# Optimization experiments

Measured on AMD Instinct MI355X. Metric: run time of the kernel, lower is better.

Reference implementation:

```python
import jax, jax.numpy as jnp
import numpy as np

N_NODES = 20000
N_EDGES = 200000
NUM_GRAPHS = 512
IN_C = 16      # in_channel
P1 = 128       # edge MLP hidden
P2 = 16        # base channel width
F_E = 16       # nbr_edge_features
C1_OUT = 3 * P2  # 48
C2_OUT = 2 * P2  # 32
C3_OUT = P2      # 16


def _nnconv(x, src, tgt, ea, W1, b1, W2, b2, root, bias, in_c, out_c):
    # edge MLP -> per-edge weight matrix [E, in_c, out_c]
    h = jax.nn.relu(ea @ W1 + b1)
    We = (h @ W2 + b2).reshape(-1, in_c, out_c)
    msg = jnp.einsum('ei,eio->eo', x[src], We)          # gather + batched matmul
    n = x.shape[0]
    agg = jax.ops.segment_sum(msg, tgt, num_segments=n)  # scatter
    deg = jax.ops.segment_sum(jnp.ones((src.shape[0],), x.dtype), tgt, num_segments=n)
    agg = agg / jnp.maximum(deg, 1.0)[:, None]           # aggr='mean'
    return agg + x @ root + bias


def _set2set(x, batch, Wih, Whh, bih, bhh, num_graphs, steps=2):
    H = x.shape[-1]
    q_star = jnp.zeros((num_graphs, 2 * H), x.dtype)
    h = jnp.zeros((num_graphs, H), x.dtype)
    c = jnp.zeros_like(h)
    for _ in range(steps):
        gates = q_star @ Wih.T + bih + h @ Whh.T + bhh   # LSTM cell (i,f,g,o)
        i, f, g, o = jnp.split(gates, 4, axis=-1)
        c = jax.nn.sigmoid(f) * c + jax.nn.sigmoid(i) * jnp.tanh(g)
        h = jax.nn.sigmoid(o) * jnp.tanh(c)
        e = jnp.sum(x * h[batch], axis=-1)               # attention logits per node
        emax = jax.ops.segment_max(e, batch, num_segments=num_graphs)
        a = jnp.exp(e - jnp.maximum(emax, -1e30)[batch])
        asum = jax.ops.segment_sum(a, batch, num_segments=num_graphs)
        a = a / jnp.maximum(asum, 1e-16)[batch]
        r = jax.ops.segment_sum(a[:, None] * x, batch, num_segments=num_graphs)
        q_star = jnp.concatenate([h, r], axis=-1)
    return q_star


def setup_inputs() -> dict:
    key = jax.random.key(0)
    ks = iter(jax.random.split(key, 40))
    d = {}
    d['x'] = jax.random.normal(next(ks), (N_NODES, IN_C), jnp.float32)
    d['edge_index'] = jax.random.randint(next(ks), (2, N_EDGES), 0, N_NODES)
    d['edge_attr'] = jax.random.uniform(next(ks), (N_EDGES, F_E), jnp.float32)
    d['batch'] = jnp.sort(jax.random.randint(next(ks), (N_NODES,), 0, NUM_GRAPHS))

    def lin(ki, fan_in, fan_out):
        s = 1.0 / np.sqrt(fan_in)
        return jax.random.uniform(ki, (fan_in, fan_out), jnp.float32, -s, s)

    for name, ic, oc in [('c1', IN_C, C1_OUT), ('c2', C1_OUT, C2_OUT), ('c3', C2_OUT, C3_OUT)]:
        d[name + '_W1'] = lin(next(ks), F_E, P1)
        d[name + '_b1'] = jnp.zeros((P1,), jnp.float32)
        d[name + '_W2'] = lin(next(ks), P1, ic * oc) * 0.1
        d[name + '_b2'] = jnp.zeros((ic * oc,), jnp.float32)
        d[name + '_root'] = lin(next(ks), ic, oc)
        d[name + '_bias'] = jnp.zeros((oc,), jnp.float32)

    H = P2
    s = 1.0 / np.sqrt(H)
    d['lstm_Wih'] = jax.random.uniform(next(ks), (4 * H, 2 * H), jnp.float32, -s, s)
    d['lstm_Whh'] = jax.random.uniform(next(ks), (4 * H, H), jnp.float32, -s, s)
    d['lstm_bih'] = jnp.zeros((4 * H,), jnp.float32)
    d['lstm_bhh'] = jnp.zeros((4 * H,), jnp.float32)

    tot = 2 * P2
    d['lin1_W'] = lin(next(ks), tot, tot // 2)
    d['lin1_b'] = jnp.zeros((tot // 2,), jnp.float32)
    d['lin2_W'] = lin(next(ks), tot // 2, tot // 4)
    d['lin2_b'] = jnp.zeros((tot // 4,), jnp.float32)
    d['linf_W'] = lin(next(ks), tot // 4, 1)
    d['linf_b'] = jnp.zeros((1,), jnp.float32)
    return d


def reference(x, edge_index, edge_attr, batch,
              c1_W1, c1_b1, c1_W2, c1_b2, c1_root, c1_bias,
              c2_W1, c2_b1, c2_W2, c2_b2, c2_root, c2_bias,
              c3_W1, c3_b1, c3_W2, c3_b2, c3_root, c3_bias,
              lstm_Wih, lstm_Whh, lstm_bih, lstm_bhh,
              lin1_W, lin1_b, lin2_W, lin2_b, linf_W, linf_b):
    src, tgt = edge_index[0], edge_index[1]
    y = jax.nn.relu(_nnconv(x, src, tgt, edge_attr, c1_W1, c1_b1, c1_W2, c1_b2, c1_root, c1_bias, IN_C, C1_OUT))
    y = jax.nn.relu(_nnconv(y, src, tgt, edge_attr, c2_W1, c2_b1, c2_W2, c2_b2, c2_root, c2_bias, C1_OUT, C2_OUT))
    y = jax.nn.relu(_nnconv(y, src, tgt, edge_attr, c3_W1, c3_b1, c3_W2, c3_b2, c3_root, c3_bias, C2_OUT, C3_OUT))
    y = _set2set(y, batch, lstm_Wih, lstm_Whh, lstm_bih, lstm_bhh, NUM_GRAPHS, steps=2)  # [B, 2*P2]
    y = jax.nn.relu(y @ lin1_W + lin1_b)
    y = jax.nn.relu(y @ lin2_W + lin2_b)
    y = (y @ linf_W + linf_b).squeeze(-1)  # [B]
    return y
```

## Files before the change

### kernel.cpp

```cpp
#include <hip/hip_runtime.h>

#define NN 20000
#define NE 200000
#define NG 512

typedef float v2f __attribute__((ext_vector_type(2)));

__device__ __forceinline__ int lowerb(const int* a, int n, int v){
  int lo=0, hi=n;
  while(lo<hi){ int m=(lo+hi)>>1; if(a[m]<v) lo=m+1; else hi=m; }
  return lo;
}

template<int AUX>
__device__ __forceinline__ void gload_lds16(const float4* g, float4* l){
  __builtin_amdgcn_global_load_lds(
    (const __attribute__((address_space(1))) void*)(g),
    (__attribute__((address_space(3))) void*)(l), 16, 0, AUX);
}

__global__ void k_count(const int* __restrict__ tgt, int* __restrict__ cnt){
  int e = blockIdx.x*blockDim.x + threadIdx.x;
  if(e<NE) atomicAdd(&cnt[tgt[e]], 1);
}

__global__ void k_scan(const int* __restrict__ cnt, int* __restrict__ row_start){
  __shared__ int part[1024];
  int t = threadIdx.x;
  const int CH = (NN + 1023)/1024;
  int i0 = t*CH;
  int s = 0;
  for(int j=0;j<CH;j++){ int i=i0+j; if(i<NN) s += cnt[i]; }
  part[t] = s; __syncthreads();
  for(int d=1; d<1024; d<<=1){
    int v = (t>=d) ? part[t-d] : 0;
    __syncthreads();
    part[t] += v;
    __syncthreads();
  }
  int run = (t==0) ? 0 : part[t-1];
  for(int j=0;j<CH;j++){ int i=i0+j; if(i<NN){ row_start[i]=run; run += cnt[i]; } }
  if(t==0) row_start[NN] = part[1023];
}

__global__ void k_place(const int* __restrict__ src, const int* __restrict__ tgt,
                        const float* __restrict__ ea,
                        const int* __restrict__ row_start, int* __restrict__ cur,
                        int* __restrict__ es_src, float* __restrict__ es_ea){
  int e = blockIdx.x*blockDim.x + threadIdx.x;
  if(e>=NE) return;
  int n = tgt[e];
  int pos = row_start[n] + atomicAdd(&cur[n],1);
  es_src[pos] = src[e];
  const float4* s = (const float4*)ea + (size_t)e*4;
  float4* d = (float4*)es_ea + (size_t)pos*4;
  d[0]=s[0]; d[1]=s[1]; d[2]=s[2]; d[3]=s[3];
}

template<int IC, int OC, int PLEN, int KS, int BN, int PP, int TI, int OQ, int TO, bool PF, int EB>
__launch_bounds__(256, 3)
__global__ void k_layer(const float* __restrict__ x_in, const float* __restrict__ es_ea,
                        const int* __restrict__ es_src, const int* __restrict__ row_start,
                        const float* __restrict__ W1, const float* __restrict__ b1,
                        const float* __restrict__ W2, float* __restrict__ part,
                        float* __restrict__ xbar_out)
{
  constexpr int K    = PLEN*IC;
  constexpr int XV   = IC/4;
  constexpr int NIW  = IC/TI;
  constexpr int NPW  = PLEN/PP;
  constexpr int G    = BN/4;
  constexpr int KQL  = 64/OQ;
  constexpr int TSPL = 4*KQL;
  constexpr int J    = (K/4)/TSPL;
  constexpr int NEA  = EB/64;
  constexpr int NX4  = (EB*XV)/256;
  constexpr int TI2  = TI/2;
  constexpr int NP   = TO/2;
  constexpr bool TODD = (TO & 1);
  constexpr int EPB  = 256/PLEN;
  static_assert(TI%2==0, "packed scatter needs even TI");
  static_assert(256%PLEN==0, "H-compute mapping");
  static_assert(EB%64==0, "ea region must be exact 256-f4 chunks");
  static_assert((EB*XV)%256==0, "xs region must be exact 256-f4 chunks");
  static_assert(EB*(PLEN+16+IC) <= BN*K, "staging alias fits in S");
  static_assert(NPW*NIW==64, "wave tile covers 64 lanes");
  static_assert(G*PP*TI <= 48, "spill-safe accumulator");
  static_assert(OQ*TO==OC && (K/4)%TSPL==0, "gemm tiling");
  static_assert(J%2==0, "ping-pong needs even J");

  __shared__ __align__(16) float S[BN*K];
  __shared__ int rs_s[BN+1], ro[BN+1];

  float* hb  = S;
  float* eas = S + EB*PLEN;
  float* xs  = S + EB*(PLEN+16);

  const int tid = threadIdx.x;
  const int wid = tid>>6, lane = tid&63;
  const int split = blockIdx.x % KS;
  const int nb = blockIdx.x / KS;
  const int n0 = nb*BN;

  if(tid<=BN) rs_s[tid] = row_start[n0+tid];
  __syncthreads();
  const int estart = rs_s[0], eend = rs_s[BN];

  const int pw = lane / NIW;
  const int iw = lane - pw*NIW;
  const int pcol = tid % PLEN, erow = tid / PLEN;

  float w1c[16];
  const float b1c = b1[split*PLEN + pcol];
  #pragma unroll
  for(int i=0;i<16;i++) w1c[i] = W1[i*128 + split*PLEN + pcol];

  v2f acc2[G][PP][TI2];
  v2f xsum2[G][TI2];
  #pragma unroll
  for(int g=0;g<G;g++){
    #pragma unroll
    for(int p=0;p<PP;p++)
      #pragma unroll
      for(int u=0;u<TI2;u++) acc2[g][p][u]=v2f{0.f,0.f};
    #pragma unroll
    for(int u=0;u<TI2;u++) xsum2[g][u]=v2f{0.f,0.f};
  }

  const float4* EA4 = (const float4*)es_ea;
  const float4* x4  = (const float4*)x_in;

  for(int bstart=estart; bstart<eend; bstart+=EB){
    const int ebc = min(EB, eend-bstart);
    if(tid<=BN){ int v = rs_s[tid]-bstart; ro[tid] = min(max(v,0), ebc); }
    const int ea_lim = ebc*4, xs_lim = ebc*XV;
    int sn_r[NX4];
    #pragma unroll
    for(int c=0;c<NX4;c++){
      int jc = min(tid + c*256, xs_lim-1);
      sn_r[c] = es_src[bstart + jc/XV];
    }
    #pragma unroll
    for(int c=0;c<NEA;c++){
      int j = tid + c*256;
      int jc = min(j, ea_lim-1);
      gload_lds16<0>(EA4 + (size_t)bstart*4 + jc, ((float4*)eas) + j);
    }
    #pragma unroll
    for(int c=0;c<NX4;c++){
      int j = tid + c*256;
      int jc = min(j, xs_lim-1);
      int q = jc - (jc/XV)*XV;
      gload_lds16<0>(x4 + (size_t)sn_r[c]*XV + q, ((float4*)xs) + j);
    }
    __syncthreads();

    for(int ec = erow; ec < ebc; ec += EPB){
      float h = b1c;
      #pragma unroll
      for(int q=0;q<4;q++){
        float4 a = *(const float4*)&eas[ec*16 + 4*q];
        h += a.x*w1c[4*q] + a.y*w1c[4*q+1] + a.z*w1c[4*q+2] + a.w*w1c[4*q+3];
      }
      hb[ec*PLEN + pcol] = fmaxf(h, 0.f);
    }
    __syncthreads();

    if constexpr (PF){
      #pragma unroll
      for(int g=0; g<G; g++){
        const int nl = wid*G + g;
        const int a = ro[nl], b = ro[nl+1];
        if(a>=b) continue;
        float hv[PP]; v2f xv2[TI2];
        #pragma unroll
        for(int p=0;p<PP;p++) hv[p] = hb[a*PLEN + pw*PP + p];
        #pragma unroll
        for(int u=0;u<TI2;u++) xv2[u] = *(const v2f*)&xs[a*IC + iw*TI + 2*u];
        for(int e=a; e<b; e++){
          float hn[PP]; v2f xn2[TI2];
          if(e+1<b){
            #pragma unroll
            for(int p=0;p<PP;p++) hn[p] = hb[(e+1)*PLEN + pw*PP + p];
            #pragma unroll
            for(int u=0;u<TI2;u++) xn2[u] = *(const v2f*)&xs[(e+1)*IC + iw*TI + 2*u];
          }
          #pragma unroll
          for(int p=0;p<PP;p++){
            v2f h2 = v2f{hv[p], hv[p]};
            #pragma unroll
            for(int u=0;u<TI2;u++) acc2[g][p][u] += h2*xv2[u];
          }
          #pragma unroll
          for(int u=0;u<TI2;u++) xsum2[g][u] += xv2[u];
          #pragma unroll
          for(int p=0;p<PP;p++) hv[p]=hn[p];
          #pragma unroll
          for(int u=0;u<TI2;u++) xv2[u]=xn2[u];
        }
      }
    } else {
      #pragma unroll
      for(int g=0; g<G; g++){
        const int nl = wid*G + g;
        const int a = ro[nl], b = ro[nl+1];
        for(int e=a; e<b; e++){
          float hv[PP];
          #pragma unroll
          for(int p=0;p<PP;p++) hv[p] = hb[e*PLEN + pw*PP + p];
          v2f xv2[TI2];
          #pragma unroll
          for(int u=0;u<TI2;u++) xv2[u] = *(const v2f*)&xs[e*IC + iw*TI + 2*u];
          #pragma unroll
          for(int p=0;p<PP;p++){
            v2f h2 = v2f{hv[p], hv[p]};
            #pragma unroll
            for(int u=0;u<TI2;u++) acc2[g][p][u] += h2*xv2[u];
          }
          #pragma unroll
          for(int u=0;u<TI2;u++) xsum2[g][u] += xv2[u];
        }
      }
    }
    __syncthreads();
  }

  if(split==0 && pw==0){
    #pragma unroll
    for(int g=0;g<G;g++){
      const int nl = wid*G + g;
      const float dv = 1.f/fmaxf((float)(rs_s[nl+1]-rs_s[nl]), 1.f);
      #pragma unroll
      for(int u=0;u<TI2;u++){
        v2f r = xsum2[g][u]*v2f{dv,dv};
        *(v2f*)&xbar_out[(size_t)(n0+nl)*IC + iw*TI + 2*u] = r;
      }
    }
  }

  #pragma unroll
  for(int g=0; g<G; g++){
    const int nl = wid*G + g;
    const float dv = 1.f/fmaxf((float)(rs_s[nl+1]-rs_s[nl]), 1.f);
    const v2f dv2 = v2f{dv, dv};
    #pragma unroll
    for(int p=0;p<PP;p++)
      #pragma unroll
      for(int u=0;u<TI2;u++)
        *(v2f*)&S[(nl*PLEN + pw*PP + p)*IC + iw*TI + 2*u] = acc2[g][p][u]*dv2;
  }

  const int oq  = lane % OQ;
  const int kql = lane / OQ;
  const int o0  = oq*TO;
  const float* W2b = W2 + (size_t)split*K*OC + o0;

  auto LOADW = [&](int j, v2f (&wv2)[4][NP], float (&wvs)[4]){
    const int k4 = j*TSPL + wid*KQL + kql;
    #pragma unroll
    for(int r=0;r<4;r++){
      const float* wr = W2b + (size_t)(4*k4+r)*OC;
      if constexpr (TO==4){
        float4 a=*(const float4*)wr;
        wv2[r][0]=v2f{a.x,a.y}; wv2[r][1]=v2f{a.z,a.w};
      } else if constexpr (TO==3){
        wv2[r][0]=v2f{wr[0],wr[1]}; wvs[r]=wr[2];
      } else {
        float2 a=*(const float2*)wr;
        wv2[r][0]=v2f{a.x,a.y};
      }
    }
  };

  v2f outp2[BN][NP];
  float outs[BN];
  #pragma unroll
  for(int n=0;n<BN;n++){
    #pragma unroll
    for(int t=0;t<NP;t++) outp2[n][t]=v2f{0.f,0.f};
    outs[n]=0.f;
  }

  v2f wvA[4][NP], wvB[4][NP];
  float wsA[4], wsB[4];
  LOADW(0, wvA, wsA);
  __syncthreads();

  #pragma unroll 1
  for(int j=0;j<J;j+=2){
    LOADW(j+1, wvB, wsB);
    {
      const int k4 = j*TSPL + wid*KQL + kql;
      #pragma unroll
      for(int n=0;n<BN;n++){
        float4 sv = *(const float4*)&S[n*K + 4*k4];
        v2f s0=v2f{sv.x,sv.x}, s1=v2f{sv.y,sv.y}, s2=v2f{sv.z,sv.z}, s3=v2f{sv.w,sv.w};
        #pragma unroll
        for(int t=0;t<NP;t++)
          outp2[n][t] += s0*wvA[0][t] + s1*wvA[1][t] + s2*wvA[2][t] + s3*wvA[3][t];
        if constexpr (TODD)
          outs[n] += sv.x*wsA[0] + sv.y*wsA[1] + sv.z*wsA[2] + sv.w*wsA[3];
      }
    }
    if(j+2<J) LOADW(j+2, wvA, wsA);
    {
      const int k4 = (j+1)*TSPL + wid*KQL + kql;
      #pragma unroll
      for(int n=0;n<BN;n++){
        float4 sv = *(const float4*)&S[n*K + 4*k4];
        v2f s0=v2f{sv.x,sv.x}, s1=v2f{sv.y,sv.y}, s2=v2f{sv.z,sv.z}, s3=v2f{sv.w,sv.w};
        #pragma unroll
        for(int t=0;t<NP;t++)
          outp2[n][t] += s0*wvB[0][t] + s1*wvB[1][t] + s2*wvB[2][t] + s3*wvB[3][t];
        if constexpr (TODD)
          outs[n] += sv.x*wsB[0] + sv.y*wsB[1] + sv.z*wsB[2] + sv.w*wsB[3];
      }
    }
  }

  #pragma unroll
  for(int m=OQ; m<64; m<<=1)
    #pragma unroll
    for(int n=0;n<BN;n++){
      #pragma unroll
      for(int t=0;t<NP;t++){
        outp2[n][t][0] += __shfl_xor(outp2[n][t][0], m, 64);
        outp2[n][t][1] += __shfl_xor(outp2[n][t][1], m, 64);
      }
      if constexpr (TODD) outs[n] += __shfl_xor(outs[n], m, 64);
    }

  if(kql==0){
    float* slice = part + (size_t)(split*4+wid)*NN*OC;
    #pragma unroll
    for(int n=0;n<BN;n++){
      float* dst = slice + (size_t)(n0+n)*OC + o0;
      if constexpr (TO==4){
        *(float4*)dst = make_float4(outp2[n][0][0],outp2[n][0][1],outp2[n][1][0],outp2[n][1][1]);
      } else if constexpr (TO==3){
        dst[0]=outp2[n][0][0]; dst[1]=outp2[n][0][1]; dst[2]=outs[n];
      } else {
        *(float2*)dst = make_float2(outp2[n][0][0],outp2[n][0][1]);
      }
    }
  }
}

template<int IC, int OC, int SL>
__global__ void k_epi(const float* __restrict__ part, const float* __restrict__ x,
                      const float* __restrict__ xbar,
                      const float* __restrict__ root, const float* __restrict__ b2,
                      const float* __restrict__ bias, float* __restrict__ y)
{
  for(int idx = blockIdx.x*256 + threadIdx.x; idx < NN*OC; idx += gridDim.x*256){
    int n = idx/OC, o = idx - n*OC;
    float v = bias[o];
    #pragma unroll
    for(int s=0;s<SL;s++) v += part[(size_t)s*NN*OC + idx];
    #pragma unroll
    for(int i=0;i<IC;i++) v += x[(size_t)n*IC+i]*root[i*OC+o];
    #pragma unroll
    for(int i=0;i<IC;i++) v += xbar[(size_t)n*IC+i]*b2[i*OC+o];
    y[idx] = fmaxf(v, 0.f);
  }
}

__global__ void k_s2s(const float* __restrict__ xg, const int* __restrict__ batch,
  const float* __restrict__ Wih, const float* __restrict__ Whh,
  const float* __restrict__ bih, const float* __restrict__ bhh,
  const float* __restrict__ l1W, const float* __restrict__ l1b,
  const float* __restrict__ l2W, const float* __restrict__ l2b,
  const float* __restrict__ lfW, const float* __restrict__ lfb,
  float* __restrict__ out)
{
  int g = blockIdx.x, lane = threadIdx.x;
  __shared__ float hs[16], cs[16], qs[32], gs[64], rs[16];
  int r0 = lowerb(batch, NN, g);
  int r1 = lowerb(batch, NN, g+1);
  if(lane<16){ hs[lane]=0.f; cs[lane]=0.f; }
  if(lane<32) qs[lane]=0.f;
  __syncthreads();
  for(int step=0; step<2; step++){
    float gate = bih[lane] + bhh[lane];
    for(int k=0;k<32;k++) gate += qs[k]*Wih[lane*32+k];
    for(int k=0;k<16;k++) gate += hs[k]*Whh[lane*16+k];
    gs[lane] = gate;
    __syncthreads();
    if(lane<16){
      float ig = 1.f/(1.f+expf(-gs[lane]));
      float fg = 1.f/(1.f+expf(-gs[lane+16]));
      float gg = tanhf(gs[lane+32]);
      float og = 1.f/(1.f+expf(-gs[lane+48]));
      float cn = fg*cs[lane] + ig*gg;
      cs[lane] = cn;
      hs[lane] = og*tanhf(cn);
    }
    __syncthreads();
    float m = -1e30f;
    for(int n=r0+lane; n<r1; n+=64){
      float e=0.f;
      for(int k=0;k<16;k++) e += xg[n*16+k]*hs[k];
      m = fmaxf(m, e);
    }
    for(int d=1; d<64; d<<=1) m = fmaxf(m, __shfl_xor(m, d));
    float ssum = 0.f;
    float racc[16];
    #pragma unroll
    for(int k=0;k<16;k++) racc[k]=0.f;
    for(int n=r0+lane; n<r1; n+=64){
      float e=0.f, xv[16];
      #pragma unroll
      for(int k=0;k<16;k++){ xv[k]=xg[n*16+k]; e += xv[k]*hs[k]; }
      float a = expf(e - m);
      ssum += a;
      #pragma unroll
      for(int k=0;k<16;k++) racc[k] += a*xv[k];
    }
    for(int d=1; d<64; d<<=1) ssum += __shfl_xor(ssum, d);
    #pragma unroll
    for(int k=0;k<16;k++)
      for(int d=1; d<64; d<<=1) racc[k] += __shfl_xor(racc[k], d);
    ssum = fmaxf(ssum, 1e-16f);
    if(lane==0){
      #pragma unroll
      for(int k=0;k<16;k++) rs[k] = racc[k]/ssum;
    }
    __syncthreads();
    if(lane<16){ qs[lane]=hs[lane]; qs[16+lane]=rs[lane]; }
    __syncthreads();
  }
  if(lane<16){
    float v = l1b[lane];
    for(int k=0;k<32;k++) v += qs[k]*l1W[k*16+lane];
    gs[lane] = fmaxf(v,0.f);
  }
  __syncthreads();
  if(lane<8){
    float v = l2b[lane];
    for(int k=0;k<16;k++) v += gs[k]*l2W[k*8+lane];
    gs[32+lane] = fmaxf(v,0.f);
  }
  __syncthreads();
  if(lane==0){
    float v = lfb[0];
    for(int k=0;k<8;k++) v += gs[32+k]*lfW[k];
    out[g] = v;
  }
}

extern "C" void kernel_launch(void* const* d_in, const int* in_sizes, int n_in,
                              void* d_out, int out_size, void* d_ws, size_t ws_size,
                              hipStream_t stream) {
  const float* x0   = (const float*)d_in[0];
  const int*   ei   = (const int*)d_in[1];
  const float* ea   = (const float*)d_in[2];
  const int*   batch= (const int*)d_in[3];
  const float* c1W1 = (const float*)d_in[4];  const float* c1b1 = (const float*)d_in[5];
  const float* c1W2 = (const float*)d_in[6];  const float* c1b2 = (const float*)d_in[7];
  const float* c1rt = (const float*)d_in[8];  const float* c1bs = (const float*)d_in[9];
  const float* c2W1 = (const float*)d_in[10]; const float* c2b1 = (const float*)d_in[11];
  const float* c2W2 = (const float*)d_in[12]; const float* c2b2 = (const float*)d_in[13];
  const float* c2rt = (const float*)d_in[14]; const float* c2bs = (const float*)d_in[15];
  const float* c3W1 = (const float*)d_in[16]; const float* c3b1 = (const float*)d_in[17];
  const float* c3W2 = (const float*)d_in[18]; const float* c3b2 = (const float*)d_in[19];
  const float* c3rt = (const float*)d_in[20]; const float* c3bs = (const float*)d_in[21];
  const float* Wih  = (const float*)d_in[22]; const float* Whh  = (const float*)d_in[23];
  const float* bih  = (const float*)d_in[24]; const float* bhh  = (const float*)d_in[25];
  const float* l1W  = (const float*)d_in[26]; const float* l1b  = (const float*)d_in[27];
  const float* l2W  = (const float*)d_in[28]; const float* l2b  = (const float*)d_in[29];
  const float* lfW  = (const float*)d_in[30]; const float* lfb  = (const float*)d_in[31];
  float* out = (float*)d_out;

  const int* src = ei;
  const int* tgt = ei + NE;

  char* w = (char*)d_ws;
  auto carve = [&](size_t bytes)->void*{ void* p = (void*)w; w += (bytes + 255) & ~(size_t)255; return p; };
  int*   row_start = (int*)carve((NN+1)*sizeof(int));
  int*   cur       = (int*)carve(NN*sizeof(int));
  int*   es_src    = (int*)carve(NE*sizeof(int));
  float* es_ea     = (float*)carve((size_t)NE*16*sizeof(float));
  float* xbar      = (float*)carve((size_t)NN*48*sizeof(float));
  float* y1   = (float*)carve((size_t)NN*48*sizeof(float));
  float* y2   = (float*)carve((size_t)NN*32*sizeof(float));
  float* y3   = (float*)carve((size_t)NN*16*sizeof(float));
  float* part = (float*)carve((size_t)16*NN*48*sizeof(float));

  hipMemsetAsync(cur, 0, NN*sizeof(int), stream);
  k_count<<<(NE+255)/256, 256, 0, stream>>>(tgt, cur);
  k_scan<<<1, 1024, 0, stream>>>(cur, row_start);
  hipMemsetAsync(cur, 0, NN*sizeof(int), stream);
  k_place<<<(NE+255)/256, 256, 0, stream>>>(src, tgt, ea, row_start, cur, es_src, es_ea);

  k_layer<16,48,64,2,8,4,4,16,3,true,64><<<(NN/8)*2, 256, 0, stream>>>(
      x0, es_ea, es_src, row_start, c1W1, c1b1, c1W2, part, xbar);
  k_epi<16,48,8><<<2048, 256, 0, stream>>>(part, x0, xbar, c1rt, c1b2, c1bs, y1);

  k_layer<48,32,32,4,8,4,6,8,4,true,128><<<(NN/8)*4, 256, 0, stream>>>(
      y1, es_ea, es_src, row_start, c2W1, c2b1, c2W2, part, xbar);
  k_epi<48,32,16><<<2048, 256, 0, stream>>>(part, y1, xbar, c2rt, c2b2, c2bs, y2);

  k_layer<32,16,64,2,4,4,8,4,4,true,64><<<(NN/4)*2, 256, 0, stream>>>(
      y2, es_ea, es_src, row_start, c3W1, c3b1, c3W2, part, xbar);
  k_epi<32,16,8><<<2048, 256, 0, stream>>>(part, y2, xbar, c3rt, c3b2, c3bs, y3);

  k_s2s<<<NG, 64, 0, stream>>>(y3, batch, Wih, Whh, bih, bhh, l1W, l1b, l2W, l2b, lfW, lfb, out);
}
```

Before: 723.5 us.

## Combine per-wave partials in LDS and pack edge-MLP hidden compute into v2f

Each block's four waves now reduce their per-node output partials through shared memory before one wave writes a single slice to global memory. This cuts the partial buffer and the epilogue's slice reads by a factor of four (8→2, 16→4, 8→2). The edge MLP hidden layer is also computed two columns per thread with packed float2 FMAs. The cost is two extra block barriers plus LDS traffic at the end of each layer kernel.

```diff
diff --git a/kernel.cpp b/kernel.cpp
--- a/kernel.cpp
+++ b/kernel.cpp
@@ -78,9 +78,10 @@
   constexpr int TI2  = TI/2;
   constexpr int NP   = TO/2;
   constexpr bool TODD = (TO & 1);
-  constexpr int EPB  = 256/PLEN;
+  constexpr int HP   = PLEN/2;
+  constexpr int EPB2 = 256/HP;
   static_assert(TI%2==0, "packed scatter needs even TI");
-  static_assert(256%PLEN==0, "H-compute mapping");
+  static_assert(256%HP==0, "packed H-compute mapping");
   static_assert(EB%64==0, "ea region must be exact 256-f4 chunks");
   static_assert((EB*XV)%256==0, "xs region must be exact 256-f4 chunks");
   static_assert(EB*(PLEN+16+IC) <= BN*K, "staging alias fits in S");
@@ -88,6 +89,7 @@
   static_assert(G*PP*TI <= 48, "spill-safe accumulator");
   static_assert(OQ*TO==OC && (K/4)%TSPL==0, "gemm tiling");
   static_assert(J%2==0, "ping-pong needs even J");
+  static_assert(3*BN*OC <= BN*K, "combine area fits in dead S");
 
   __shared__ __align__(16) float S[BN*K];
   __shared__ int rs_s[BN+1], ro[BN+1];
@@ -108,12 +110,12 @@
 
   const int pw = lane / NIW;
   const int iw = lane - pw*NIW;
-  const int pcol = tid % PLEN, erow = tid / PLEN;
-
-  float w1c[16];
-  const float b1c = b1[split*PLEN + pcol];
+  const int c2 = tid % HP, erow = tid / HP;
+
+  v2f w1cp[16];
+  const v2f b1cp = *(const v2f*)&b1[split*PLEN + 2*c2];
   #pragma unroll
-  for(int i=0;i<16;i++) w1c[i] = W1[i*128 + split*PLEN + pcol];
+  for(int i=0;i<16;i++) w1cp[i] = *(const v2f*)&W1[i*128 + split*PLEN + 2*c2];
 
   v2f acc2[G][PP][TI2];
   v2f xsum2[G][TI2];
@@ -155,14 +157,18 @@
     }
     __syncthreads();
 
-    for(int ec = erow; ec < ebc; ec += EPB){
-      float h = b1c;
+    for(int ec = erow; ec < ebc; ec += EPB2){
+      v2f h = b1cp;
       #pragma unroll
       for(int q=0;q<4;q++){
         float4 a = *(const float4*)&eas[ec*16 + 4*q];
-        h += a.x*w1c[4*q] + a.y*w1c[4*q+1] + a.z*w1c[4*q+2] + a.w*w1c[4*q+3];
-      }
-      hb[ec*PLEN + pcol] = fmaxf(h, 0.f);
+        h += v2f{a.x,a.x}*w1cp[4*q+0];
+        h += v2f{a.y,a.y}*w1cp[4*q+1];
+        h += v2f{a.z,a.z}*w1cp[4*q+2];
+        h += v2f{a.w,a.w}*w1cp[4*q+3];
+      }
+      h[0] = fmaxf(h[0],0.f); h[1] = fmaxf(h[1],0.f);
+      *(v2f*)&hb[ec*PLEN + 2*c2] = h;
     }
     __syncthreads();
 
@@ -330,17 +336,38 @@
       if constexpr (TODD) outs[n] += __shfl_xor(outs[n], m, 64);
     }
 
-  if(kql==0){
-    float* slice = part + (size_t)(split*4+wid)*NN*OC;
+  __syncthreads();
+  if(wid>0 && kql==0){
     #pragma unroll
     for(int n=0;n<BN;n++){
+      #pragma unroll
+      for(int t=0;t<NP;t++){
+        S[((wid-1)*BN+n)*OC + o0 + 2*t]   = outp2[n][t][0];
+        S[((wid-1)*BN+n)*OC + o0 + 2*t+1] = outp2[n][t][1];
+      }
+      if constexpr (TODD) S[((wid-1)*BN+n)*OC + o0 + TO-1] = outs[n];
+    }
+  }
+  __syncthreads();
+  if(wid==0 && kql==0){
+    float* slice = part + (size_t)split*NN*OC;
+    #pragma unroll
+    for(int n=0;n<BN;n++){
+      float tmp[TO];
+      #pragma unroll
+      for(int t=0;t<NP;t++){ tmp[2*t]=outp2[n][t][0]; tmp[2*t+1]=outp2[n][t][1]; }
+      if constexpr (TODD) tmp[TO-1]=outs[n];
+      #pragma unroll
+      for(int w2=0;w2<3;w2++)
+        #pragma unroll
+        for(int t=0;t<TO;t++) tmp[t] += S[(w2*BN+n)*OC + o0 + t];
       float* dst = slice + (size_t)(n0+n)*OC + o0;
       if constexpr (TO==4){
-        *(float4*)dst = make_float4(outp2[n][0][0],outp2[n][0][1],outp2[n][1][0],outp2[n][1][1]);
+        *(float4*)dst = make_float4(tmp[0],tmp[1],tmp[2],tmp[3]);
       } else if constexpr (TO==3){
-        dst[0]=outp2[n][0][0]; dst[1]=outp2[n][0][1]; dst[2]=outs[n];
+        dst[0]=tmp[0]; dst[1]=tmp[1]; dst[2]=tmp[2];
       } else {
-        *(float2*)dst = make_float2(outp2[n][0][0],outp2[n][0][1]);
+        *(float2*)dst = make_float2(tmp[0],tmp[1]);
       }
     }
   }
@@ -494,15 +521,15 @@
 
   k_layer<16,48,64,2,8,4,4,16,3,true,64><<<(NN/8)*2, 256, 0, stream>>>(
       x0, es_ea, es_src, row_start, c1W1, c1b1, c1W2, part, xbar);
-  k_epi<16,48,8><<<2048, 256, 0, stream>>>(part, x0, xbar, c1rt, c1b2, c1bs, y1);
+  k_epi<16,48,2><<<2048, 256, 0, stream>>>(part, x0, xbar, c1rt, c1b2, c1bs, y1);
 
   k_layer<48,32,32,4,8,4,6,8,4,true,128><<<(NN/8)*4, 256, 0, stream>>>(
       y1, es_ea, es_src, row_start, c2W1, c2b1, c2W2, part, xbar);
-  k_epi<48,32,16><<<2048, 256, 0, stream>>>(part, y1, xbar, c2rt, c2b2, c2bs, y2);
+  k_epi<48,32,4><<<2048, 256, 0, stream>>>(part, y1, xbar, c2rt, c2b2, c2bs, y2);
 
   k_layer<32,16,64,2,4,4,8,4,4,true,64><<<(NN/4)*2, 256, 0, stream>>>(
       y2, es_ea, es_src, row_start, c3W1, c3b1, c3W2, part, xbar);
-  k_epi<32,16,8><<<2048, 256, 0, stream>>>(part, y2, xbar, c3rt, c3b2, c3bs, y3);
+  k_epi<32,16,2><<<2048, 256, 0, stream>>>(part, y2, xbar, c3rt, c3b2, c3bs, y3);
 
   k_s2s<<<NG, 64, 0, stream>>>(y3, batch, Wih, Whh, bih, bhh, l1W, l1b, l2W, l2b, lfW, lfb, out);
 }
```

Measured after the change: 690.0 us (median of 2 runs). 4.6% less time.
